# Kernel tuning notes

Hardware: AMD Instinct MI355X
Metric: run time of the kernel (lower is better)

The kernel has to match this reference:

```python
import jax, jax.numpy as jnp
import numpy as np

H = 16
K = 64

def setup_inputs() -> dict:
    key = jax.random.key(0)
    k1, k2, k3 = jax.random.split(key, 3)
    b, m, d = 8, 1024, 1024
    x = jax.random.normal(k1, (b, m, d), dtype=jnp.float32)
    P_i = jax.random.normal(k2, (d, 3 * d), dtype=jnp.float32) * (1.0 / np.sqrt(d))
    P_o = jax.random.normal(k3, (d, d), dtype=jnp.float32) * (1.0 / np.sqrt(d))
    return {"x": x, "P_i": P_i, "P_o": P_o}

def reference(x, P_i, P_o):
    b, m, d = x.shape
    # fused QKV projection: [b, m, 3d] -> [b, m, h, 3k] -> [b, h, m, 3k]
    t = (x @ P_i).reshape(b, m, H, 3 * K).transpose(0, 2, 1, 3)
    Q, Kt, V = t[..., :K], t[..., K:2 * K], t[..., 2 * K:]
    logits = jnp.einsum('bhmk,bhnk->bhmn', Q, Kt) / jnp.sqrt(jnp.float32(K))
    # causal mask (tril): position m attends to n <= m
    causal = jnp.tril(jnp.ones((m, m), dtype=bool))
    logits = jnp.where(causal[None, None], logits, jnp.float32(-jnp.inf))
    w = jax.nn.softmax(logits, axis=-1)
    o = jnp.einsum('bhmn,bhnk->bhmk', w, V)  # [b, h, m, k]
    y = o.transpose(0, 2, 1, 3).reshape(b, m, H * K) @ P_o
    return y
```

## Files before the change

kernel.cpp:

```cpp
#include <hip/hip_runtime.h>

typedef unsigned short u16;
typedef __bf16 b16x8_t __attribute__((ext_vector_type(8)));
typedef unsigned short u16x8 __attribute__((ext_vector_type(8)));
typedef float f32x4 __attribute__((ext_vector_type(4)));

__device__ __forceinline__ u16 f2bf(float f) {
  union { float f; unsigned u; } x; x.f = f;
  unsigned r = x.u + 0x7fffu + ((x.u >> 16) & 1u);
  return (u16)(r >> 16);
}

__device__ __forceinline__ f32x4 mfma16(u16x8 a, u16x8 b, f32x4 c) {
  return __builtin_amdgcn_mfma_f32_16x16x32_bf16(
      __builtin_bit_cast(b16x8_t, a), __builtin_bit_cast(b16x8_t, b), c, 0, 0, 0);
}

__device__ __forceinline__ void gld_lds16(const void* g, void* l) {
  __builtin_amdgcn_global_load_lds(
      (const __attribute__((address_space(1))) void*)g,
      (__attribute__((address_space(3))) void*)l, 16, 0, 0);
}

__device__ __forceinline__ void store_out(float* p, float v) { *p = v; }
__device__ __forceinline__ void store_out(u16* p, float v) { *p = f2bf(v); }

__global__ void convert_bf16(const float* __restrict__ src, u16* __restrict__ dst, int n4) {
  int i = blockIdx.x * blockDim.x + threadIdx.x;
  if (i < n4) {
    float4 f = ((const float4*)src)[i];
    u16 a0 = f2bf(f.x), a1 = f2bf(f.y), a2 = f2bf(f.z), a3 = f2bf(f.w);
    unsigned lo = (unsigned)a0 | ((unsigned)a1 << 16);
    unsigned hi = (unsigned)a2 | ((unsigned)a3 << 16);
    ((uint2*)dst)[i] = make_uint2(lo, hi);
  }
}

__global__ void transpose_f32_bf16(const float* __restrict__ src, u16* __restrict__ dst,
                                   int R, int Cn) {
  __shared__ float t[32][33];
  int c0 = blockIdx.x * 32, r0 = blockIdx.y * 32;
  int tx = threadIdx.x, ty = threadIdx.y;
  for (int j = 0; j < 32; j += 8)
    t[ty + j][tx] = src[(size_t)(r0 + ty + j) * Cn + c0 + tx];
  __syncthreads();
  for (int j = 0; j < 32; j += 8)
    dst[(size_t)(c0 + ty + j) * R + r0 + tx] = f2bf(t[tx][ty + j]);
}

template <typename OutT, int BN, int EPI>
__global__ __launch_bounds__(256, 2) void gemm_v7(const u16* __restrict__ A,
                                                  const u16* __restrict__ Bt,
                                                  OutT* __restrict__ C,
                                                  u16* __restrict__ Vt,
                                                  int M, int N, int K) {
  constexpr int NB = BN / 64;
  constexpr int NJ = BN / 32;
  constexpr int NL = 2 + NB;
  __shared__ __align__(16) u16 sA[3][4096];
  __shared__ __align__(16) u16 sB[3][BN * 32];
  const int tid = threadIdx.x, lane = tid & 63, wid = tid >> 6;
  const int hi = lane >> 4, ln = lane & 15;
  const int wm = (wid >> 1) * 64, wn = (wid & 1) * (BN / 2);

  const int gdx = gridDim.x;
  const int nwg = gdx * gridDim.y;
  int wg = blockIdx.y * gdx + blockIdx.x;
  wg = (wg & 7) * (nwg >> 3) + (wg >> 3);
  const int m0 = (wg / gdx) * 128;
  const int n0 = (wg % gdx) * BN;

  const int sr = tid >> 2;
  const int scsw = ((tid & 3) ^ ((tid >> 3) & 3)) * 8;
  const u16* srcA = A + (size_t)(m0 + sr) * K + scsw;
  const u16* srcB = Bt + (size_t)(n0 + sr) * K + scsw;
  const size_t K64 = (size_t)64 * K;

  auto stage = [&](int buf, int t) {
    const int k0 = t * 32;
    gld_lds16(srcA + k0, &sA[buf][tid * 8]);
    gld_lds16(srcA + K64 + k0, &sA[buf][2048 + tid * 8]);
    gld_lds16(srcB + k0, &sB[buf][tid * 8]);
    gld_lds16(srcB + K64 + k0, &sB[buf][2048 + tid * 8]);
    if (NB > 2) gld_lds16(srcB + 2 * K64 + k0, &sB[buf][4096 + tid * 8]);
  };

  const int csw = (hi ^ ((ln >> 1) & 3)) * 8;
  int offA[4], offB[NJ];
#pragma unroll
  for (int i = 0; i < 4; ++i) offA[i] = (wm + i * 16 + ln) * 32 + csw;
#pragma unroll
  for (int j = 0; j < NJ; ++j) offB[j] = (wn + j * 16 + ln) * 32 + csw;

  f32x4 acc[4][NJ] = {};
  const int NT = K >> 5;

  stage(0, 0); stage(1, 1);
  if constexpr (NL == 5) asm volatile("s_waitcnt vmcnt(5)" ::: "memory");
  else                   asm volatile("s_waitcnt vmcnt(4)" ::: "memory");
  __builtin_amdgcn_s_barrier();

  int cb = 0, sb = 2;
  for (int kt = 0; kt < NT; ++kt) {
    u16x8 af[4], bf[NJ];
#pragma unroll
    for (int i = 0; i < 4; ++i) af[i] = *(const u16x8*)(&sA[cb][offA[i]]);
#pragma unroll
    for (int j = 0; j < NJ; ++j) bf[j] = *(const u16x8*)(&sB[cb][offB[j]]);
    if (kt + 2 < NT) {
      stage(sb, kt + 2);
      sb = (sb == 2) ? 0 : sb + 1;
      if constexpr (NL == 5) asm volatile("s_waitcnt vmcnt(5)" ::: "memory");
      else                   asm volatile("s_waitcnt vmcnt(4)" ::: "memory");
    } else {
      asm volatile("s_waitcnt vmcnt(0)" ::: "memory");
    }
    __builtin_amdgcn_s_barrier();
    asm volatile("s_waitcnt lgkmcnt(0)" ::: "memory");
    __builtin_amdgcn_sched_barrier(0);
    __builtin_amdgcn_s_setprio(1);
#pragma unroll
    for (int i = 0; i < 4; ++i)
#pragma unroll
      for (int j = 0; j < NJ; ++j)
        acc[i][j] = mfma16(af[i], bf[j], acc[i][j]);
    __builtin_amdgcn_s_setprio(0);
    __builtin_amdgcn_sched_barrier(0);
    __builtin_amdgcn_s_barrier();
    cb = (cb == 2) ? 0 : cb + 1;
  }

#pragma unroll
  for (int i = 0; i < 4; ++i) {
    int rr = m0 + wm + i * 16 + hi * 4;
#pragma unroll
    for (int j = 0; j < NJ; ++j) {
      int colw = wn + j * 16 + ln;
      if (EPI == 1 && colw >= 128) {
        int h = n0 / 192, kk = colw - 128;
        int b = rr >> 10, n = rr & 1023;
        ushort4 pk;
        pk.x = f2bf(acc[i][j][0]); pk.y = f2bf(acc[i][j][1]);
        pk.z = f2bf(acc[i][j][2]); pk.w = f2bf(acc[i][j][3]);
        *(ushort4*)(Vt + ((size_t)(b * 16 + h) * 64 + kk) * 1024 + n) = pk;
      } else {
        float sc = (EPI == 1 && colw < 64) ? 0.125f : 1.f;
        int col = n0 + colw;
#pragma unroll
        for (int r = 0; r < 4; ++r)
          store_out(&C[(size_t)(rr + r) * N + col], acc[i][j][r] * sc);
      }
    }
  }
}

__global__ __launch_bounds__(512, 6) void attn_fwd5(const u16* __restrict__ QKV,
                                                    const u16* __restrict__ Vt,
                                                    u16* __restrict__ O) {
  __shared__ __align__(16) u16 sK[2][4096];
  __shared__ __align__(16) u16 sVt[2][4096];
  __shared__ __align__(16) u16 sP[8][16 * 72];
  const int tid = threadIdx.x, lane = tid & 63, wid = tid >> 6;
  const int z = blockIdx.x, h = blockIdx.y, bb = blockIdx.z;
  const size_t rowbase = (size_t)bb * 1024;
  const size_t vbase = ((size_t)bb * 16 + h) * 64;
  const int colQ = h * 192, colK = colQ + 64;
  const int hi = lane >> 4, ln = lane & 15;
  const int slr = lane >> 3;
  const int sle = ((lane & 7) ^ slr) * 8;
  u16* sPw = sP[wid];
  const u16x8 onesf = {0x3F80, 0x3F80, 0x3F80, 0x3F80, 0x3F80, 0x3F80, 0x3F80, 0x3F80};

  auto stageKV = [&](int buf, int nt) {
    const int n0g = nt * 64;
    gld_lds16(QKV + (rowbase + n0g + 8 * wid + slr) * 3072 + colK + sle,
              &sK[buf][wid * 512]);
    gld_lds16(Vt + (vbase + 8 * wid + slr) * 1024 + n0g + sle,
              &sVt[buf][wid * 512]);
  };

  for (int half = 0; half < 2; ++half) {
    const int mt = half ? (7 - z) : z;
    const int qrow0 = mt * 128 + wid * 16;
    const int ntiles = 2 * mt + 2;

    u16x8 qf[2];
#pragma unroll
    for (int kb = 0; kb < 2; ++kb)
      qf[kb] = *(const u16x8*)(QKV + (rowbase + qrow0 + ln) * 3072 + colQ + kb * 32 + hi * 8);

    f32x4 o[4] = {};
    f32x4 lacc = {0.f, 0.f, 0.f, 0.f};

    stageKV(0, 0);
    for (int nt = 0; nt < ntiles; ++nt) {
      __syncthreads();
      if (nt + 1 < ntiles) stageKV((nt + 1) & 1, nt + 1);
      const int buf = nt & 1;
      const int n0g = nt * 64;
      if (n0g <= qrow0 + 15) {
        f32x4 s[4] = {};
        __builtin_amdgcn_s_setprio(1);
#pragma unroll
        for (int kb = 0; kb < 2; ++kb)
#pragma unroll
          for (int j = 0; j < 4; ++j) {
            int row = j * 16 + ln;
            int cb = (kb * 64 + hi * 16) ^ ((row & 7) << 4);
            u16x8 kfr = *(const u16x8*)(&sK[buf][(row * 128 + cb) >> 1]);
            s[j] = mfma16(qf[kb], kfr, s[j]);
          }
        __builtin_amdgcn_s_setprio(0);
        if (n0g + 63 > qrow0) {
#pragma unroll
          for (int j = 0; j < 4; ++j) {
            int col = n0g + j * 16 + ln;
#pragma unroll
            for (int r = 0; r < 4; ++r)
              if (col > qrow0 + hi * 4 + r) s[j][r] = -3e38f;
          }
        }
#pragma unroll
        for (int j = 0; j < 4; ++j)
#pragma unroll
          for (int r = 0; r < 4; ++r)
            sPw[(hi * 4 + r) * 72 + j * 16 + ln] = f2bf(__expf(s[j][r]));
        u16x8 pf[2];
#pragma unroll
        for (int kb2 = 0; kb2 < 2; ++kb2)
          pf[kb2] = *(const u16x8*)(&sPw[ln * 72 + kb2 * 32 + hi * 8]);
        __builtin_amdgcn_s_setprio(1);
        lacc = mfma16(pf[0], onesf, lacc);
        lacc = mfma16(pf[1], onesf, lacc);
#pragma unroll
        for (int dt = 0; dt < 4; ++dt)
#pragma unroll
          for (int kb2 = 0; kb2 < 2; ++kb2) {
            int row = dt * 16 + ln;
            int cb = (kb2 * 64 + hi * 16) ^ ((row & 7) << 4);
            u16x8 vfr = *(const u16x8*)(&sVt[buf][(row * 128 + cb) >> 1]);
            o[dt] = mfma16(pf[kb2], vfr, o[dt]);
          }
        __builtin_amdgcn_s_setprio(0);
      }
    }
#pragma unroll
    for (int r = 0; r < 4; ++r) {
      float inv = 1.f / lacc[r];
#pragma unroll
      for (int dt = 0; dt < 4; ++dt)
        O[(rowbase + qrow0 + hi * 4 + r) * 1024 + h * 64 + dt * 16 + ln] =
            f2bf(o[dt][r] * inv);
    }
  }
}

extern "C" void kernel_launch(void* const* d_in, const int* in_sizes, int n_in,
                              void* d_out, int out_size, void* d_ws, size_t ws_size,
                              hipStream_t stream) {
  const float* x = (const float*)d_in[0];
  const float* Pi = (const float*)d_in[1];
  const float* Po = (const float*)d_in[2];
  float* y = (float*)d_out;
  char* ws = (char*)d_ws;

  u16* qkv  = (u16*)(ws);
  u16* piT  = (u16*)(ws + 50331648);
  u16* poT  = (u16*)(ws + 56623104);
  u16* xbf  = (u16*)(ws + 58720256);
  u16* vt   = (u16*)(ws + 75497472);
  u16* obuf = (u16*)(ws + 58720256);

  convert_bf16<<<8192, 256, 0, stream>>>(x, xbf, 8388608 / 4);
  dim3 tb(32, 8);
  transpose_f32_bf16<<<dim3(96, 32), tb, 0, stream>>>(Pi, piT, 1024, 3072);
  transpose_f32_bf16<<<dim3(32, 32), tb, 0, stream>>>(Po, poT, 1024, 1024);

  gemm_v7<u16, 192, 1><<<dim3(16, 64), 256, 0, stream>>>(xbf, piT, qkv, vt,
                                                         8192, 3072, 1024);
  attn_fwd5<<<dim3(4, 16, 8), 512, 0, stream>>>(qkv, vt, obuf);
  gemm_v7<float, 128, 0><<<dim3(8, 64), 256, 0, stream>>>(obuf, poT, y, nullptr,
                                                          8192, 1024, 1024);
}
```

Before: 143.7 us.

## Process both paired query tiles in one KV sweep to share K/V loads

Attention now handles the two complementary query tiles (z and 7-z) in a single loop over KV tiles instead of two sequential passes. Each staged K/V tile is reused by both query tiles, so the short tile's KV loads and barriers are no longer issued a second time. This doubles the accumulator registers per thread, and the launch bound's minimum-occupancy hint drops from 6 to 4 to allow for that. The risk is lower occupancy and the extra register pressure.

```diff
diff --git a/kernel.cpp b/kernel.cpp
--- a/kernel.cpp
+++ b/kernel.cpp
@@ -154,7 +154,7 @@
   }
 }
 
-__global__ __launch_bounds__(512, 6) void attn_fwd5(const u16* __restrict__ QKV,
+__global__ __launch_bounds__(512, 4) void attn_fwd6(const u16* __restrict__ QKV,
                                                     const u16* __restrict__ Vt,
                                                     u16* __restrict__ O) {
   __shared__ __align__(16) u16 sK[2][4096];
@@ -179,78 +179,88 @@
               &sVt[buf][wid * 512]);
   };
 
-  for (int half = 0; half < 2; ++half) {
-    const int mt = half ? (7 - z) : z;
-    const int qrow0 = mt * 128 + wid * 16;
-    const int ntiles = 2 * mt + 2;
-
-    u16x8 qf[2];
+  const int mtA = z, mtB = 7 - z;
+  const int qrow0A = mtA * 128 + wid * 16;
+  const int qrow0B = mtB * 128 + wid * 16;
+  const int ntA = 2 * mtA + 2, ntB = 2 * mtB + 2;
+
+  u16x8 qfA[2], qfB[2];
+#pragma unroll
+  for (int kb = 0; kb < 2; ++kb) {
+    qfA[kb] = *(const u16x8*)(QKV + (rowbase + qrow0A + ln) * 3072 + colQ + kb * 32 + hi * 8);
+    qfB[kb] = *(const u16x8*)(QKV + (rowbase + qrow0B + ln) * 3072 + colQ + kb * 32 + hi * 8);
+  }
+
+  f32x4 oA[4] = {}, oB[4] = {};
+  f32x4 laccA = {0.f, 0.f, 0.f, 0.f}, laccB = {0.f, 0.f, 0.f, 0.f};
+
+  auto computeHalf = [&](const u16x8* qf, f32x4* o, f32x4& lacc, int qrow0,
+                         int buf, int n0g) {
+    f32x4 s[4] = {};
+    __builtin_amdgcn_s_setprio(1);
 #pragma unroll
     for (int kb = 0; kb < 2; ++kb)
-      qf[kb] = *(const u16x8*)(QKV + (rowbase + qrow0 + ln) * 3072 + colQ + kb * 32 + hi * 8);
-
-    f32x4 o[4] = {};
-    f32x4 lacc = {0.f, 0.f, 0.f, 0.f};
-
-    stageKV(0, 0);
-    for (int nt = 0; nt < ntiles; ++nt) {
-      __syncthreads();
-      if (nt + 1 < ntiles) stageKV((nt + 1) & 1, nt + 1);
-      const int buf = nt & 1;
-      const int n0g = nt * 64;
-      if (n0g <= qrow0 + 15) {
-        f32x4 s[4] = {};
-        __builtin_amdgcn_s_setprio(1);
-#pragma unroll
-        for (int kb = 0; kb < 2; ++kb)
-#pragma unroll
-          for (int j = 0; j < 4; ++j) {
-            int row = j * 16 + ln;
-            int cb = (kb * 64 + hi * 16) ^ ((row & 7) << 4);
-            u16x8 kfr = *(const u16x8*)(&sK[buf][(row * 128 + cb) >> 1]);
-            s[j] = mfma16(qf[kb], kfr, s[j]);
-          }
-        __builtin_amdgcn_s_setprio(0);
-        if (n0g + 63 > qrow0) {
-#pragma unroll
-          for (int j = 0; j < 4; ++j) {
-            int col = n0g + j * 16 + ln;
-#pragma unroll
-            for (int r = 0; r < 4; ++r)
-              if (col > qrow0 + hi * 4 + r) s[j][r] = -3e38f;
-          }
-        }
-#pragma unroll
-        for (int j = 0; j < 4; ++j)
-#pragma unroll
-          for (int r = 0; r < 4; ++r)
-            sPw[(hi * 4 + r) * 72 + j * 16 + ln] = f2bf(__expf(s[j][r]));
-        u16x8 pf[2];
-#pragma unroll
-        for (int kb2 = 0; kb2 < 2; ++kb2)
-          pf[kb2] = *(const u16x8*)(&sPw[ln * 72 + kb2 * 32 + hi * 8]);
-        __builtin_amdgcn_s_setprio(1);
-        lacc = mfma16(pf[0], onesf, lacc);
-        lacc = mfma16(pf[1], onesf, lacc);
-#pragma unroll
-        for (int dt = 0; dt < 4; ++dt)
-#pragma unroll
-          for (int kb2 = 0; kb2 < 2; ++kb2) {
-            int row = dt * 16 + ln;
-            int cb = (kb2 * 64 + hi * 16) ^ ((row & 7) << 4);
-            u16x8 vfr = *(const u16x8*)(&sVt[buf][(row * 128 + cb) >> 1]);
-            o[dt] = mfma16(pf[kb2], vfr, o[dt]);
-          }
-        __builtin_amdgcn_s_setprio(0);
-      }
-    }
-#pragma unroll
-    for (int r = 0; r < 4; ++r) {
-      float inv = 1.f / lacc[r];
-#pragma unroll
-      for (int dt = 0; dt < 4; ++dt)
-        O[(rowbase + qrow0 + hi * 4 + r) * 1024 + h * 64 + dt * 16 + ln] =
-            f2bf(o[dt][r] * inv);
+#pragma unroll
+      for (int j = 0; j < 4; ++j) {
+        int row = j * 16 + ln;
+        int cb = (kb * 64 + hi * 16) ^ ((row & 7) << 4);
+        u16x8 kfr = *(const u16x8*)(&sK[buf][(row * 128 + cb) >> 1]);
+        s[j] = mfma16(qf[kb], kfr, s[j]);
+      }
+    __builtin_amdgcn_s_setprio(0);
+    if (n0g + 63 > qrow0) {
+#pragma unroll
+      for (int j = 0; j < 4; ++j) {
+        int col = n0g + j * 16 + ln;
+#pragma unroll
+        for (int r = 0; r < 4; ++r)
+          if (col > qrow0 + hi * 4 + r) s[j][r] = -3e38f;
+      }
+    }
+#pragma unroll
+    for (int j = 0; j < 4; ++j)
+#pragma unroll
+      for (int r = 0; r < 4; ++r)
+        sPw[(hi * 4 + r) * 72 + j * 16 + ln] = f2bf(__expf(s[j][r]));
+    u16x8 pf[2];
+#pragma unroll
+    for (int kb2 = 0; kb2 < 2; ++kb2)
+      pf[kb2] = *(const u16x8*)(&sPw[ln * 72 + kb2 * 32 + hi * 8]);
+    __builtin_amdgcn_s_setprio(1);
+    lacc = mfma16(pf[0], onesf, lacc);
+    lacc = mfma16(pf[1], onesf, lacc);
+#pragma unroll
+    for (int dt = 0; dt < 4; ++dt)
+#pragma unroll
+      for (int kb2 = 0; kb2 < 2; ++kb2) {
+        int row = dt * 16 + ln;
+        int cb = (kb2 * 64 + hi * 16) ^ ((row & 7) << 4);
+        u16x8 vfr = *(const u16x8*)(&sVt[buf][(row * 128 + cb) >> 1]);
+        o[dt] = mfma16(pf[kb2], vfr, o[dt]);
+      }
+    __builtin_amdgcn_s_setprio(0);
+  };
+
+  stageKV(0, 0);
+  for (int nt = 0; nt < ntB; ++nt) {
+    __syncthreads();
+    if (nt + 1 < ntB) stageKV((nt + 1) & 1, nt + 1);
+    const int buf = nt & 1;
+    const int n0g = nt * 64;
+    if (nt < ntA && n0g <= qrow0A + 15) computeHalf(qfA, oA, laccA, qrow0A, buf, n0g);
+    if (n0g <= qrow0B + 15)             computeHalf(qfB, oB, laccB, qrow0B, buf, n0g);
+  }
+
+#pragma unroll
+  for (int r = 0; r < 4; ++r) {
+    float invA = 1.f / laccA[r];
+    float invB = 1.f / laccB[r];
+#pragma unroll
+    for (int dt = 0; dt < 4; ++dt) {
+      O[(rowbase + qrow0A + hi * 4 + r) * 1024 + h * 64 + dt * 16 + ln] =
+          f2bf(oA[dt][r] * invA);
+      O[(rowbase + qrow0B + hi * 4 + r) * 1024 + h * 64 + dt * 16 + ln] =
+          f2bf(oB[dt][r] * invB);
     }
   }
 }
@@ -278,7 +288,7 @@
 
   gemm_v7<u16, 192, 1><<<dim3(16, 64), 256, 0, stream>>>(xbf, piT, qkv, vt,
                                                          8192, 3072, 1024);
-  attn_fwd5<<<dim3(4, 16, 8), 512, 0, stream>>>(qkv, vt, obuf);
+  attn_fwd6<<<dim3(4, 16, 8), 512, 0, stream>>>(qkv, vt, obuf);
   gemm_v7<float, 128, 0><<<dim3(8, 64), 256, 0, stream>>>(obuf, poT, y, nullptr,
                                                           8192, 1024, 1024);
 }
```

Result: faster. 138.2 us (-3.8%).
